# Optimization experiments

Measured on AMD Instinct MI355X. Metric: run time of the kernel, lower is better.

Reference implementation:

```python
import jax, jax.numpy as jnp
import numpy as np

T, IN, H, OUT = 512, 1024, 2048, 1024


def setup_inputs() -> dict:
    key = jax.random.key(0)
    ks = jax.random.split(key, 13)
    s = 0.02
    return {
        "word": jax.random.normal(ks[0], (T, 1, IN), dtype=jnp.float32),
        "W_i2h1": jax.random.normal(ks[1], (H, IN), dtype=jnp.float32) * s,
        "b_i2h1": jax.random.normal(ks[2], (H,), dtype=jnp.float32) * s,
        "W_h2h1": jax.random.normal(ks[3], (H, H), dtype=jnp.float32) * s,
        "b_h2h1": jax.random.normal(ks[4], (H,), dtype=jnp.float32) * s,
        "W_h2o1": jax.random.normal(ks[5], (OUT, H), dtype=jnp.float32) * s,
        "b_h2o1": jax.random.normal(ks[6], (OUT,), dtype=jnp.float32) * s,
        "W_i2h2": jax.random.normal(ks[7], (H, H), dtype=jnp.float32) * s,
        "b_i2h2": jax.random.normal(ks[8], (H,), dtype=jnp.float32) * s,
        "W_h2h2": jax.random.normal(ks[9], (H, H), dtype=jnp.float32) * s,
        "b_h2h2": jax.random.normal(ks[10], (H,), dtype=jnp.float32) * s,
        "W_h2o2": jax.random.normal(ks[11], (OUT, H), dtype=jnp.float32) * s,
        "b_h2o2": jax.random.normal(ks[12], (OUT,), dtype=jnp.float32) * s,
    }


def reference(word, W_i2h1, b_i2h1, W_h2h1, b_h2h1, W_h2o1, b_h2o1,
              W_i2h2, b_i2h2, W_h2h2, b_h2h2, W_h2o2, b_h2o2):
    # 2-layer vanilla tanh RNN; layer2's input is layer1's hidden state.
    # layer1's h2o projection is computed-but-unused in the original module
    # (dead code), so it is omitted from the live dataflow here.
    hidden_dtype = word.dtype
    h1_0 = jnp.zeros((1, W_h2h1.shape[0]), dtype=hidden_dtype)
    h2_0 = jnp.zeros((1, W_h2h2.shape[0]), dtype=hidden_dtype)

    def step(carry, x):  # x: [1, IN]
        h1, h2 = carry
        h1 = jnp.tanh(x @ W_i2h1.T + b_i2h1 + h1 @ W_h2h1.T + b_h2h1)
        h2 = jnp.tanh(h1 @ W_i2h2.T + b_i2h2 + h2 @ W_h2h2.T + b_h2h2)
        return (h1, h2), None

    (h1, h2), _ = jax.lax.scan(step, (h1_0, h2_0), word)
    # output of the final step only
    return h2 @ W_h2o2.T + b_h2o2
```

## Files before the change

kernel.cpp:

```cpp
#include <hip/hip_runtime.h>

#define TT   512
#define DIN  1024
#define DH   2048
#define DOUT 1024

#define NWG   256
#define HALF  128
#define NTHR  512
#define NSLOT (TT + 1)

typedef unsigned int u32;
typedef unsigned long long u64;

__device__ u64 gR1[NSLOT * DH];
__device__ u64 gR2[NSLOT * DH];
__device__ u32 g_epoch_base;

__device__ __forceinline__ float dot4(float4 a, float4 b) {
  return a.x * b.x + a.y * b.y + a.z * b.z + a.w * b.w;
}
__device__ __forceinline__ float wave_sum(float v) {
  #pragma unroll
  for (int off = 32; off > 0; off >>= 1) v += __shfl_down(v, off, 64);
  return v;
}
__device__ __forceinline__ u64 ld_rec(const u64* p) {
  return __hip_atomic_load((u64*)p, __ATOMIC_RELAXED, __HIP_MEMORY_SCOPE_AGENT);
}
__device__ __forceinline__ void st_rec(u64* p, u64 v) {
  __hip_atomic_store(p, v, __ATOMIC_RELAXED, __HIP_MEMORY_SCOPE_AGENT);
}
__device__ __forceinline__ u64 pack(float h, u32 ep) {
  return ((u64)ep << 32) | (u64)__float_as_uint(h);
}
__device__ __forceinline__ float fast_tanh(float x) {
  float xc = fminf(fmaxf(x, -9.0f), 9.0f);
  float e  = __expf(2.0f * xc);
  return (e - 1.0f) * __frcp_rn(e + 1.0f);
}

__device__ __forceinline__ void poll_stage(const u64* rec, u32 ep,
                                           float* lds, int tid) {
  u64 v0 = 0, v1 = 0, v2 = 0, v3 = 0;
  bool d0 = false, d1 = false, d2 = false, d3 = false;
  for (;;) {
    if (!d0) { v0 = ld_rec(rec + tid           ); d0 = ((u32)(v0 >> 32) == ep); }
    if (!d1) { v1 = ld_rec(rec + tid +     NTHR); d1 = ((u32)(v1 >> 32) == ep); }
    if (!d2) { v2 = ld_rec(rec + tid + 2 * NTHR); d2 = ((u32)(v2 >> 32) == ep); }
    if (!d3) { v3 = ld_rec(rec + tid + 3 * NTHR); d3 = ((u32)(v3 >> 32) == ep); }
    if (d0 & d1 & d2 & d3) break;
    __builtin_amdgcn_s_sleep(1);
  }
  lds[tid           ] = __uint_as_float((u32)v0);
  lds[tid +     NTHR] = __uint_as_float((u32)v1);
  lds[tid + 2 * NTHR] = __uint_as_float((u32)v2);
  lds[tid + 3 * NTHR] = __uint_as_float((u32)v3);
}

__device__ __forceinline__ void poll_stage2(const u64* recA, u32 epA,
                                            const u64* recB, u32 epB,
                                            float* ldsA, float* ldsB, int tid) {
  u64 a0 = 0, a1 = 0, a2 = 0, a3 = 0, b0 = 0, b1 = 0, b2 = 0, b3 = 0;
  bool da0 = false, da1 = false, da2 = false, da3 = false;
  bool db0 = false, db1 = false, db2 = false, db3 = false;
  for (;;) {
    if (!da0) { a0 = ld_rec(recA + tid           ); da0 = ((u32)(a0 >> 32) == epA); }
    if (!da1) { a1 = ld_rec(recA + tid +     NTHR); da1 = ((u32)(a1 >> 32) == epA); }
    if (!da2) { a2 = ld_rec(recA + tid + 2 * NTHR); da2 = ((u32)(a2 >> 32) == epA); }
    if (!da3) { a3 = ld_rec(recA + tid + 3 * NTHR); da3 = ((u32)(a3 >> 32) == epA); }
    if (!db0) { b0 = ld_rec(recB + tid           ); db0 = ((u32)(b0 >> 32) == epB); }
    if (!db1) { b1 = ld_rec(recB + tid +     NTHR); db1 = ((u32)(b1 >> 32) == epB); }
    if (!db2) { b2 = ld_rec(recB + tid + 2 * NTHR); db2 = ((u32)(b2 >> 32) == epB); }
    if (!db3) { b3 = ld_rec(recB + tid + 3 * NTHR); db3 = ((u32)(b3 >> 32) == epB); }
    if (da0 & da1 & da2 & da3 & db0 & db1 & db2 & db3) break;
    __builtin_amdgcn_s_sleep(1);
  }
  ldsA[tid           ] = __uint_as_float((u32)a0);
  ldsA[tid +     NTHR] = __uint_as_float((u32)a1);
  ldsA[tid + 2 * NTHR] = __uint_as_float((u32)a2);
  ldsA[tid + 3 * NTHR] = __uint_as_float((u32)a3);
  ldsB[tid           ] = __uint_as_float((u32)b0);
  ldsB[tid +     NTHR] = __uint_as_float((u32)b1);
  ldsB[tid + 2 * NTHR] = __uint_as_float((u32)b2);
  ldsB[tid + 3 * NTHR] = __uint_as_float((u32)b3);
}

__global__ void bump_kernel() {
  if (threadIdx.x == 0)
    __hip_atomic_fetch_add(&g_epoch_base, (u32)NSLOT,
                           __ATOMIC_RELAXED, __HIP_MEMORY_SCOPE_AGENT);
}

__global__ __launch_bounds__(NTHR, 2)
void rnn2_kernel(const float* __restrict__ X,
                 const float* __restrict__ Wa, const float* __restrict__ ba,
                 const float* __restrict__ Wb, const float* __restrict__ bb,
                 const float* __restrict__ Wc, const float* __restrict__ bc,
                 const float* __restrict__ Wd, const float* __restrict__ bd,
                 const float* __restrict__ Wo, const float* __restrict__ bo,
                 float* __restrict__ out)
{
  const int g   = blockIdx.x;
  const int tid = threadIdx.x;
  const int w   = tid >> 6;
  const int l   = tid & 63;

  const u32 eb = __hip_atomic_load(&g_epoch_base, __ATOMIC_RELAXED,
                                   __HIP_MEMORY_SCOPE_AGENT);

  __shared__ float sA[2][DH];
  __shared__ float sB[2][DH];

  if (g < HALF) {
    const int r0 = g * 16 + 2 * w, r1 = r0 + 1;
    float4 wA0[4], wA1[4], wB0[8], wB1[8], wO[8];
    {
      const float4* p0 = (const float4*)(Wa + (size_t)r0 * DIN);
      const float4* p1 = (const float4*)(Wa + (size_t)r1 * DIN);
      #pragma unroll
      for (int j = 0; j < 4; ++j) { wA0[j] = p0[l + 64 * j]; wA1[j] = p1[l + 64 * j]; }
    }
    {
      const float4* p0 = (const float4*)(Wb + (size_t)r0 * DH);
      const float4* p1 = (const float4*)(Wb + (size_t)r1 * DH);
      #pragma unroll
      for (int j = 0; j < 8; ++j) { wB0[j] = p0[l + 64 * j]; wB1[j] = p1[l + 64 * j]; }
    }
    const int orow = g * 8 + w;
    {
      const float4* p = (const float4*)(Wo + (size_t)orow * DH);
      #pragma unroll
      for (int j = 0; j < 8; ++j) wO[j] = p[l + 64 * j];
    }
    const float b1_0 = ba[r0] + bb[r0];
    const float b1_1 = ba[r1] + bb[r1];
    const float bo_r = bo[orow];

    for (int t = 1; t <= TT; ++t) {
      float a0 = 0.f, a1 = 0.f;
      {
        const float4* px = (const float4*)(X + (size_t)(t - 1) * DIN);
        #pragma unroll
        for (int j = 0; j < 4; ++j) {
          float4 x4 = px[l + 64 * j];
          a0 += dot4(wA0[j], x4);
          a1 += dot4(wA1[j], x4);
        }
      }
      if (t > 1) {
        float* buf = sA[(t - 1) & 1];
        poll_stage(gR1 + (size_t)(t - 1) * DH, eb + (u32)(t - 1), buf, tid);
        __syncthreads();
        const float4* ph = (const float4*)buf;
        #pragma unroll
        for (int j = 0; j < 8; ++j) {
          float4 h4 = ph[l + 64 * j];
          a0 += dot4(wB0[j], h4);
          a1 += dot4(wB1[j], h4);
        }
      }
      a0 = wave_sum(a0); a1 = wave_sum(a1);
      if (l == 0) {
        u64* dst = gR1 + (size_t)t * DH;
        st_rec(dst + r0, pack(fast_tanh(a0 + b1_0), eb + (u32)t));
        st_rec(dst + r1, pack(fast_tanh(a1 + b1_1), eb + (u32)t));
      }
    }

    poll_stage(gR2 + (size_t)TT * DH, eb + (u32)TT, sA[0], tid);
    __syncthreads();
    {
      const float4* ph = (const float4*)sA[0];
      float acc = 0.f;
      #pragma unroll
      for (int j = 0; j < 8; ++j) acc += dot4(wO[j], ph[l + 64 * j]);
      acc = wave_sum(acc);
      if (l == 0) out[orow] = acc + bo_r;
    }
  } else {
    const int gg = g - HALF;
    const int r0 = gg * 16 + 2 * w, r1 = r0 + 1;
    float4 wC0[8], wC1[8], wD0[8], wD1[8];
    {
      const float4* p0 = (const float4*)(Wc + (size_t)r0 * DH);
      const float4* p1 = (const float4*)(Wc + (size_t)r1 * DH);
      #pragma unroll
      for (int j = 0; j < 8; ++j) { wC0[j] = p0[l + 64 * j]; wC1[j] = p1[l + 64 * j]; }
    }
    {
      const float4* p0 = (const float4*)(Wd + (size_t)r0 * DH);
      const float4* p1 = (const float4*)(Wd + (size_t)r1 * DH);
      #pragma unroll
      for (int j = 0; j < 8; ++j) { wD0[j] = p0[l + 64 * j]; wD1[j] = p1[l + 64 * j]; }
    }
    const float b2_0 = bc[r0] + bd[r0];
    const float b2_1 = bc[r1] + bd[r1];

    for (int t = 1; t <= TT; ++t) {
      float* bufA = sA[t & 1];
      float* bufB = sB[t & 1];
      if (t > 1)
        poll_stage2(gR1 + (size_t)t * DH, eb + (u32)t,
                    gR2 + (size_t)(t - 1) * DH, eb + (u32)(t - 1), bufA, bufB, tid);
      else
        poll_stage(gR1 + (size_t)t * DH, eb + (u32)t, bufA, tid);
      __syncthreads();

      float a0 = 0.f, a1 = 0.f;
      {
        const float4* ph = (const float4*)bufA;
        #pragma unroll
        for (int j = 0; j < 8; ++j) {
          float4 h4 = ph[l + 64 * j];
          a0 += dot4(wC0[j], h4);
          a1 += dot4(wC1[j], h4);
        }
      }
      if (t > 1) {
        const float4* ph = (const float4*)bufB;
        #pragma unroll
        for (int j = 0; j < 8; ++j) {
          float4 h4 = ph[l + 64 * j];
          a0 += dot4(wD0[j], h4);
          a1 += dot4(wD1[j], h4);
        }
      }
      a0 = wave_sum(a0); a1 = wave_sum(a1);
      if (l == 0) {
        u64* dst = gR2 + (size_t)t * DH;
        st_rec(dst + r0, pack(fast_tanh(a0 + b2_0), eb + (u32)t));
        st_rec(dst + r1, pack(fast_tanh(a1 + b2_1), eb + (u32)t));
      }
    }
  }
}

extern "C" void kernel_launch(void* const* d_in, const int* in_sizes, int n_in,
                              void* d_out, int out_size, void* d_ws, size_t ws_size,
                              hipStream_t stream)
{
  (void)in_sizes; (void)n_in; (void)out_size; (void)d_ws; (void)ws_size;

  const float* X  = (const float*)d_in[0];
  const float* Wa = (const float*)d_in[1];
  const float* ba = (const float*)d_in[2];
  const float* Wb = (const float*)d_in[3];
  const float* bb = (const float*)d_in[4];
  const float* Wc = (const float*)d_in[7];
  const float* bc = (const float*)d_in[8];
  const float* Wd = (const float*)d_in[9];
  const float* bd = (const float*)d_in[10];
  const float* Wo = (const float*)d_in[11];
  const float* bo = (const float*)d_in[12];
  float* out = (float*)d_out;

  bump_kernel<<<dim3(1), dim3(64), 0, stream>>>();

  void* args[] = { &X, &Wa, &ba, &Wb, &bb, &Wc, &bc, &Wd, &bd, &Wo, &bo, &out };
  (void)hipLaunchCooperativeKernel((void*)rnn2_kernel, dim3(NWG), dim3(NTHR),
                                   args, 0, stream);
}
```

Baseline: 1.570 ms.

## Add per-workgroup ready flags and bulk vectorized staging of hidden state

Each workgroup now counts its 8 finished waves with an LDS atomic, and the last one publishes a per-workgroup epoch flag. Consumers make one wave poll 128 flags instead of having all threads spin on 2048 tagged records. After the flags are seen, the hidden vector is read with vectorized 16-byte loads, and the per-record epoch check is kept as a fallback for ordering. This is meant to cut polling traffic on the L2 and the contention in each timestep handoff, at the cost of an extra flag store and an extra barrier per step. The flag and data stores are both relaxed, so the code relies on the record-level retry loop for correctness.

```diff
diff --git a/kernel.cpp b/kernel.cpp
--- a/kernel.cpp
+++ b/kernel.cpp
@@ -15,6 +15,8 @@
 
 __device__ u64 gR1[NSLOT * DH];
 __device__ u64 gR2[NSLOT * DH];
+__device__ u32 gF1[NSLOT * HALF];
+__device__ u32 gF2[NSLOT * HALF];
 __device__ u32 g_epoch_base;
 
 __device__ __forceinline__ float dot4(float4 a, float4 b) {
@@ -31,6 +33,12 @@
 __device__ __forceinline__ void st_rec(u64* p, u64 v) {
   __hip_atomic_store(p, v, __ATOMIC_RELAXED, __HIP_MEMORY_SCOPE_AGENT);
 }
+__device__ __forceinline__ u32 ld_flag(const u32* p) {
+  return __hip_atomic_load((u32*)p, __ATOMIC_RELAXED, __HIP_MEMORY_SCOPE_AGENT);
+}
+__device__ __forceinline__ void st_flag(u32* p, u32 v) {
+  __hip_atomic_store(p, v, __ATOMIC_RELAXED, __HIP_MEMORY_SCOPE_AGENT);
+}
 __device__ __forceinline__ u64 pack(float h, u32 ep) {
   return ((u64)ep << 32) | (u64)__float_as_uint(h);
 }
@@ -40,50 +48,85 @@
   return (e - 1.0f) * __frcp_rn(e + 1.0f);
 }
 
-__device__ __forceinline__ void poll_stage(const u64* rec, u32 ep,
+__device__ __forceinline__ void poll_flags(const u32* f, u32 ep, int tid) {
+  if (tid < 64) {
+    bool d0 = false, d1 = false;
+    for (;;) {
+      if (!d0) d0 = (ld_flag(f + tid     ) == ep);
+      if (!d1) d1 = (ld_flag(f + tid + 64) == ep);
+      if (d0 & d1) break;
+      __builtin_amdgcn_s_sleep(1);
+    }
+  }
+  __syncthreads();
+}
+__device__ __forceinline__ void poll_flags2(const u32* fA, u32 epA,
+                                            const u32* fB, u32 epB, int tid) {
+  if (tid < 64) {
+    bool a0 = false, a1 = false, b0 = false, b1 = false;
+    for (;;) {
+      if (!a0) a0 = (ld_flag(fA + tid     ) == epA);
+      if (!a1) a1 = (ld_flag(fA + tid + 64) == epA);
+      if (!b0) b0 = (ld_flag(fB + tid     ) == epB);
+      if (!b1) b1 = (ld_flag(fB + tid + 64) == epB);
+      if (a0 & a1 & b0 & b1) break;
+      __builtin_amdgcn_s_sleep(1);
+    }
+  }
+  __syncthreads();
+}
+
+__device__ __forceinline__ void bulk_stage(const u64* rec, u32 ep,
                                            float* lds, int tid) {
-  u64 v0 = 0, v1 = 0, v2 = 0, v3 = 0;
-  bool d0 = false, d1 = false, d2 = false, d3 = false;
-  for (;;) {
-    if (!d0) { v0 = ld_rec(rec + tid           ); d0 = ((u32)(v0 >> 32) == ep); }
-    if (!d1) { v1 = ld_rec(rec + tid +     NTHR); d1 = ((u32)(v1 >> 32) == ep); }
-    if (!d2) { v2 = ld_rec(rec + tid + 2 * NTHR); d2 = ((u32)(v2 >> 32) == ep); }
-    if (!d3) { v3 = ld_rec(rec + tid + 3 * NTHR); d3 = ((u32)(v3 >> 32) == ep); }
-    if (d0 & d1 & d2 & d3) break;
+  const u64* p = rec + 4 * (size_t)tid;
+  const ulonglong2* q = (const ulonglong2*)p;
+  ulonglong2 q0 = q[0], q1 = q[1];
+  u64 v0 = q0.x, v1 = q0.y, v2 = q1.x, v3 = q1.y;
+  bool d0 = ((u32)(v0 >> 32) == ep), d1 = ((u32)(v1 >> 32) == ep);
+  bool d2 = ((u32)(v2 >> 32) == ep), d3 = ((u32)(v3 >> 32) == ep);
+  while (!(d0 & d1 & d2 & d3)) {
     __builtin_amdgcn_s_sleep(1);
-  }
-  lds[tid           ] = __uint_as_float((u32)v0);
-  lds[tid +     NTHR] = __uint_as_float((u32)v1);
-  lds[tid + 2 * NTHR] = __uint_as_float((u32)v2);
-  lds[tid + 3 * NTHR] = __uint_as_float((u32)v3);
-}
-
-__device__ __forceinline__ void poll_stage2(const u64* recA, u32 epA,
+    if (!d0) { v0 = ld_rec(p + 0); d0 = ((u32)(v0 >> 32) == ep); }
+    if (!d1) { v1 = ld_rec(p + 1); d1 = ((u32)(v1 >> 32) == ep); }
+    if (!d2) { v2 = ld_rec(p + 2); d2 = ((u32)(v2 >> 32) == ep); }
+    if (!d3) { v3 = ld_rec(p + 3); d3 = ((u32)(v3 >> 32) == ep); }
+  }
+  ((float4*)lds)[tid] = make_float4(
+      __uint_as_float((u32)v0), __uint_as_float((u32)v1),
+      __uint_as_float((u32)v2), __uint_as_float((u32)v3));
+}
+
+__device__ __forceinline__ void bulk_stage2(const u64* recA, u32 epA,
                                             const u64* recB, u32 epB,
                                             float* ldsA, float* ldsB, int tid) {
-  u64 a0 = 0, a1 = 0, a2 = 0, a3 = 0, b0 = 0, b1 = 0, b2 = 0, b3 = 0;
-  bool da0 = false, da1 = false, da2 = false, da3 = false;
-  bool db0 = false, db1 = false, db2 = false, db3 = false;
-  for (;;) {
-    if (!da0) { a0 = ld_rec(recA + tid           ); da0 = ((u32)(a0 >> 32) == epA); }
-    if (!da1) { a1 = ld_rec(recA + tid +     NTHR); da1 = ((u32)(a1 >> 32) == epA); }
-    if (!da2) { a2 = ld_rec(recA + tid + 2 * NTHR); da2 = ((u32)(a2 >> 32) == epA); }
-    if (!da3) { a3 = ld_rec(recA + tid + 3 * NTHR); da3 = ((u32)(a3 >> 32) == epA); }
-    if (!db0) { b0 = ld_rec(recB + tid           ); db0 = ((u32)(b0 >> 32) == epB); }
-    if (!db1) { b1 = ld_rec(recB + tid +     NTHR); db1 = ((u32)(b1 >> 32) == epB); }
-    if (!db2) { b2 = ld_rec(recB + tid + 2 * NTHR); db2 = ((u32)(b2 >> 32) == epB); }
-    if (!db3) { b3 = ld_rec(recB + tid + 3 * NTHR); db3 = ((u32)(b3 >> 32) == epB); }
-    if (da0 & da1 & da2 & da3 & db0 & db1 & db2 & db3) break;
+  const u64* pa = recA + 4 * (size_t)tid;
+  const u64* pb = recB + 4 * (size_t)tid;
+  const ulonglong2* qa = (const ulonglong2*)pa;
+  const ulonglong2* qb = (const ulonglong2*)pb;
+  ulonglong2 a01 = qa[0], a23 = qa[1], b01 = qb[0], b23 = qb[1];
+  u64 a0 = a01.x, a1 = a01.y, a2 = a23.x, a3 = a23.y;
+  u64 b0 = b01.x, b1 = b01.y, b2 = b23.x, b3 = b23.y;
+  bool da0 = ((u32)(a0 >> 32) == epA), da1 = ((u32)(a1 >> 32) == epA);
+  bool da2 = ((u32)(a2 >> 32) == epA), da3 = ((u32)(a3 >> 32) == epA);
+  bool db0 = ((u32)(b0 >> 32) == epB), db1 = ((u32)(b1 >> 32) == epB);
+  bool db2 = ((u32)(b2 >> 32) == epB), db3 = ((u32)(b3 >> 32) == epB);
+  while (!(da0 & da1 & da2 & da3 & db0 & db1 & db2 & db3)) {
     __builtin_amdgcn_s_sleep(1);
-  }
-  ldsA[tid           ] = __uint_as_float((u32)a0);
-  ldsA[tid +     NTHR] = __uint_as_float((u32)a1);
-  ldsA[tid + 2 * NTHR] = __uint_as_float((u32)a2);
-  ldsA[tid + 3 * NTHR] = __uint_as_float((u32)a3);
-  ldsB[tid           ] = __uint_as_float((u32)b0);
-  ldsB[tid +     NTHR] = __uint_as_float((u32)b1);
-  ldsB[tid + 2 * NTHR] = __uint_as_float((u32)b2);
-  ldsB[tid + 3 * NTHR] = __uint_as_float((u32)b3);
+    if (!da0) { a0 = ld_rec(pa + 0); da0 = ((u32)(a0 >> 32) == epA); }
+    if (!da1) { a1 = ld_rec(pa + 1); da1 = ((u32)(a1 >> 32) == epA); }
+    if (!da2) { a2 = ld_rec(pa + 2); da2 = ((u32)(a2 >> 32) == epA); }
+    if (!da3) { a3 = ld_rec(pa + 3); da3 = ((u32)(a3 >> 32) == epA); }
+    if (!db0) { b0 = ld_rec(pb + 0); db0 = ((u32)(b0 >> 32) == epB); }
+    if (!db1) { b1 = ld_rec(pb + 1); db1 = ((u32)(b1 >> 32) == epB); }
+    if (!db2) { b2 = ld_rec(pb + 2); db2 = ((u32)(b2 >> 32) == epB); }
+    if (!db3) { b3 = ld_rec(pb + 3); db3 = ((u32)(b3 >> 32) == epB); }
+  }
+  ((float4*)ldsA)[tid] = make_float4(
+      __uint_as_float((u32)a0), __uint_as_float((u32)a1),
+      __uint_as_float((u32)a2), __uint_as_float((u32)a3));
+  ((float4*)ldsB)[tid] = make_float4(
+      __uint_as_float((u32)b0), __uint_as_float((u32)b1),
+      __uint_as_float((u32)b2), __uint_as_float((u32)b3));
 }
 
 __global__ void bump_kernel() {
@@ -111,6 +154,9 @@
 
   __shared__ float sA[2][DH];
   __shared__ float sB[2][DH];
+  __shared__ u32 sDone[2];
+  if (tid == 0) { sDone[0] = 0u; sDone[1] = 0u; }
+  __syncthreads();
 
   if (g < HALF) {
     const int r0 = g * 16 + 2 * w, r1 = r0 + 1;
@@ -149,8 +195,10 @@
         }
       }
       if (t > 1) {
+        const u32 epp = eb + (u32)(t - 1);
         float* buf = sA[(t - 1) & 1];
-        poll_stage(gR1 + (size_t)(t - 1) * DH, eb + (u32)(t - 1), buf, tid);
+        poll_flags(gF1 + (size_t)(t - 1) * HALF, epp, tid);
+        bulk_stage(gR1 + (size_t)(t - 1) * DH, epp, buf, tid);
         __syncthreads();
         const float4* ph = (const float4*)buf;
         #pragma unroll
@@ -162,15 +210,23 @@
       }
       a0 = wave_sum(a0); a1 = wave_sum(a1);
       if (l == 0) {
+        const u32 ept = eb + (u32)t;
         u64* dst = gR1 + (size_t)t * DH;
-        st_rec(dst + r0, pack(fast_tanh(a0 + b1_0), eb + (u32)t));
-        st_rec(dst + r1, pack(fast_tanh(a1 + b1_1), eb + (u32)t));
-      }
-    }
-
-    poll_stage(gR2 + (size_t)TT * DH, eb + (u32)TT, sA[0], tid);
-    __syncthreads();
-    {
+        st_rec(dst + r0, pack(fast_tanh(a0 + b1_0), ept));
+        st_rec(dst + r1, pack(fast_tanh(a1 + b1_1), ept));
+        u32 old = atomicAdd(&sDone[t & 1], 1u);
+        if (old == 7u) {
+          sDone[t & 1] = 0u;
+          st_flag(&gF1[(size_t)t * HALF + g], ept);
+        }
+      }
+    }
+
+    {
+      const u32 epT = eb + (u32)TT;
+      poll_flags(gF2 + (size_t)TT * HALF, epT, tid);
+      bulk_stage(gR2 + (size_t)TT * DH, epT, sA[0], tid);
+      __syncthreads();
       const float4* ph = (const float4*)sA[0];
       float acc = 0.f;
       #pragma unroll
@@ -200,11 +256,17 @@
     for (int t = 1; t <= TT; ++t) {
       float* bufA = sA[t & 1];
       float* bufB = sB[t & 1];
-      if (t > 1)
-        poll_stage2(gR1 + (size_t)t * DH, eb + (u32)t,
-                    gR2 + (size_t)(t - 1) * DH, eb + (u32)(t - 1), bufA, bufB, tid);
-      else
-        poll_stage(gR1 + (size_t)t * DH, eb + (u32)t, bufA, tid);
+      const u32 ept = eb + (u32)t;
+      if (t > 1) {
+        const u32 epp = eb + (u32)(t - 1);
+        poll_flags2(gF1 + (size_t)t * HALF, ept,
+                    gF2 + (size_t)(t - 1) * HALF, epp, tid);
+        bulk_stage2(gR1 + (size_t)t * DH, ept,
+                    gR2 + (size_t)(t - 1) * DH, epp, bufA, bufB, tid);
+      } else {
+        poll_flags(gF1 + (size_t)1 * HALF, eb + 1u, tid);
+        bulk_stage(gR1 + (size_t)1 * DH, eb + 1u, bufA, tid);
+      }
       __syncthreads();
 
       float a0 = 0.f, a1 = 0.f;
@@ -229,8 +291,13 @@
       a0 = wave_sum(a0); a1 = wave_sum(a1);
       if (l == 0) {
         u64* dst = gR2 + (size_t)t * DH;
-        st_rec(dst + r0, pack(fast_tanh(a0 + b2_0), eb + (u32)t));
-        st_rec(dst + r1, pack(fast_tanh(a1 + b2_1), eb + (u32)t));
+        st_rec(dst + r0, pack(fast_tanh(a0 + b2_0), ept));
+        st_rec(dst + r1, pack(fast_tanh(a1 + b2_1), ept));
+        u32 old = atomicAdd(&sDone[t & 1], 1u);
+        if (old == 7u) {
+          sDone[t & 1] = 0u;
+          st_flag(&gF2[(size_t)t * HALF + gg], ept);
+        }
       }
     }
   }
```

Result: slower. 1.984 ms (+26.4%).
